# Performance work log

Measured on AMD Instinct MI355X. Metric: run time of the kernel, lower is better.

The kernel has to match this reference:

```python
import jax, jax.numpy as jnp
import numpy as np

HEADS = 16
KV_HEADS = 4
HEAD_DIM = 64
EMBED = 1024


def setup_inputs() -> dict:
    key = jax.random.key(0)
    k1, k2, k3, k4, k5 = jax.random.split(key, 5)
    B, S, G, E = 1, 2048, 2, EMBED
    scale = 1.0 / np.sqrt(E)
    x = jax.random.normal(k1, (B, S, G, E), dtype=jnp.float32)
    Wq = jax.random.normal(k2, (E, HEADS * HEAD_DIM), dtype=jnp.float32) * scale
    Wk = jax.random.normal(k3, (E, KV_HEADS * HEAD_DIM), dtype=jnp.float32) * scale
    Wv = jax.random.normal(k4, (E, KV_HEADS * HEAD_DIM), dtype=jnp.float32) * scale
    Wo = jax.random.normal(k5, (E, E), dtype=jnp.float32) * scale
    return {"x": x, "Wq": Wq, "Wk": Wk, "Wv": Wv, "Wo": Wo}


def reference(x, Wq, Wk, Wv, Wo):
    B, S, G, E = x.shape
    ratio = HEADS // KV_HEADS
    # projections over last dim (no bias, no activation)
    q = (x @ Wq).reshape(B, S, G, HEADS, HEAD_DIM)
    k = (x @ Wk).reshape(B, S, G, KV_HEADS, HEAD_DIM)
    v = (x @ Wv).reshape(B, S, G, KV_HEADS, HEAD_DIM)
    # GQA repeat_kv: each kv head repeated `ratio` times consecutively
    k = jnp.repeat(k, ratio, axis=3)  # [B,S,G,H,D]
    v = jnp.repeat(v, ratio, axis=3)
    # energy: [B,G,H,Q,K]
    energy = jnp.einsum('bqghd,bkghd->bghqk', q, k)
    # causal mask: triu(1) set to -inf (before the sqrt scaling, as in source)
    causal = jnp.triu(jnp.ones((S, S), dtype=bool), 1)
    energy = jnp.where(causal, -jnp.inf, energy)
    scores = jax.nn.softmax(energy / np.sqrt(HEAD_DIM), axis=-1)
    attn = jnp.einsum('bghqv,bvghd->bqghd', scores, v)
    attn = attn.reshape(B, S, G, E)
    return attn @ Wo
```

## Files before the change

kernel.cpp:

```cpp
#include <hip/hip_runtime.h>
#include <cstdint>
#include <cstddef>

typedef __bf16 bf16_t;
typedef bf16_t bf16x8 __attribute__((ext_vector_type(8)));
typedef float f32x4 __attribute__((ext_vector_type(4)));

__device__ inline bf16x8 load8(const float* p) {
  f32x4 a = *reinterpret_cast<const f32x4*>(p);
  f32x4 b = *reinterpret_cast<const f32x4*>(p + 4);
  bf16x8 r;
  r[0] = (bf16_t)a[0]; r[1] = (bf16_t)a[1];
  r[2] = (bf16_t)a[2]; r[3] = (bf16_t)a[3];
  r[4] = (bf16_t)b[0]; r[5] = (bf16_t)b[1];
  r[6] = (bf16_t)b[2]; r[7] = (bf16_t)b[3];
  return r;
}
__device__ inline bf16x8 load8(const bf16_t* p) {
  return *reinterpret_cast<const bf16x8*>(p);
}

__global__ __launch_bounds__(256) void cvtx_k(const float* __restrict__ x,
                                              bf16_t* __restrict__ xb) {
  const size_t i = (size_t)blockIdx.x * 2048 + (size_t)threadIdx.x * 8;
  *reinterpret_cast<bf16x8*>(xb + i) = load8(x + i);
}

__global__ __launch_bounds__(256) void cvtT_k(
    const float* __restrict__ Wq, const float* __restrict__ Wk,
    const float* __restrict__ Wv, const float* __restrict__ Wo,
    bf16_t* __restrict__ wqT, bf16_t* __restrict__ wkT,
    bf16_t* __restrict__ wvT, bf16_t* __restrict__ woT) {
  __shared__ bf16_t Ts[64][72];
  const int b = blockIdx.x;
  const float* S;
  bf16_t* D;
  int N, idx;
  if (b < 256) { S = Wq; D = wqT; N = 1024; idx = b; }
  else if (b < 320) { S = Wk; D = wkT; N = 256; idx = b - 256; }
  else if (b < 384) { S = Wv; D = wvT; N = 256; idx = b - 320; }
  else { S = Wo; D = woT; N = 1024; idx = b - 384; }
  const int ntl = (N == 1024) ? 4 : 2;
  const int kt0 = (idx >> ntl) * 64;
  const int n0 = (idx & ((1 << ntl) - 1)) * 64;
  const int tid = threadIdx.x;
#pragma unroll
  for (int i = 0; i < 2; ++i) {
    const int c = tid + 256 * i;
    const int row = c >> 3, col0 = (c & 7) * 8;
    *reinterpret_cast<bf16x8*>(&Ts[row][col0]) =
        load8(&S[(size_t)(kt0 + row) * N + n0 + col0]);
  }
  __syncthreads();
#pragma unroll
  for (int i = 0; i < 2; ++i) {
    const int c = tid + 256 * i;
    const int nrow = c >> 3, k0 = (c & 7) * 8;
    bf16x8 v;
#pragma unroll
    for (int j = 0; j < 8; ++j) v[j] = Ts[k0 + j][nrow];
    *reinterpret_cast<bf16x8*>(&D[(size_t)(n0 + nrow) * 1024 + kt0 + k0]) = v;
  }
}

template <typename OutT>
__device__ inline void gemm_bt_body(const bf16_t* __restrict__ A,
                                    const bf16_t* __restrict__ BT,
                                    OutT* __restrict__ C, int m0, int bt0,
                                    int K, int CN, int cn0, float alpha) {
  __shared__ __align__(16) bf16_t As[128][40];
  __shared__ __align__(16) bf16_t Bs[128][40];

  const int tid = threadIdx.x;
  const int wave = tid >> 6, lane = tid & 63;
  const int quad = lane >> 4, l16 = lane & 15;
  const int moff = (wave & 1) * 64, noff = (wave >> 1) * 64;

  f32x4 acc[4][4];
#pragma unroll
  for (int mt = 0; mt < 4; ++mt)
#pragma unroll
    for (int nt = 0; nt < 4; ++nt) acc[mt][nt] = {0.f, 0.f, 0.f, 0.f};

  const int arow = tid >> 1, ak0 = (tid & 1) * 16;

  bf16x8 a0, a1, b0, b1;
  {
    const bf16_t* ap = &A[(size_t)(m0 + arow) * K + ak0];
    a0 = load8(ap); a1 = load8(ap + 8);
    const bf16_t* bp = &BT[(size_t)(bt0 + arow) * K + ak0];
    b0 = load8(bp); b1 = load8(bp + 8);
  }

  for (int k0 = 0; k0 < K; k0 += 32) {
    *reinterpret_cast<bf16x8*>(&As[arow][ak0]) = a0;
    *reinterpret_cast<bf16x8*>(&As[arow][ak0 + 8]) = a1;
    *reinterpret_cast<bf16x8*>(&Bs[arow][ak0]) = b0;
    *reinterpret_cast<bf16x8*>(&Bs[arow][ak0 + 8]) = b1;
    __syncthreads();
    if (k0 + 32 < K) {
      const bf16_t* ap = &A[(size_t)(m0 + arow) * K + k0 + 32 + ak0];
      a0 = load8(ap); a1 = load8(ap + 8);
      const bf16_t* bp = &BT[(size_t)(bt0 + arow) * K + k0 + 32 + ak0];
      b0 = load8(bp); b1 = load8(bp + 8);
    }
    bf16x8 af[4], bfr[4];
#pragma unroll
    for (int mt = 0; mt < 4; ++mt)
      af[mt] =
          *reinterpret_cast<const bf16x8*>(&As[moff + mt * 16 + l16][quad * 8]);
#pragma unroll
    for (int nt = 0; nt < 4; ++nt)
      bfr[nt] =
          *reinterpret_cast<const bf16x8*>(&Bs[noff + nt * 16 + l16][quad * 8]);
#pragma unroll
    for (int mt = 0; mt < 4; ++mt)
#pragma unroll
      for (int nt = 0; nt < 4; ++nt)
        acc[mt][nt] = __builtin_amdgcn_mfma_f32_16x16x32_bf16(
            af[mt], bfr[nt], acc[mt][nt], 0, 0, 0);
    __syncthreads();
  }

#pragma unroll
  for (int mt = 0; mt < 4; ++mt) {
    const int crow = m0 + moff + mt * 16 + quad * 4;
#pragma unroll
    for (int nt = 0; nt < 4; ++nt) {
      const int ccol = cn0 + noff + nt * 16 + l16;
#pragma unroll
      for (int r = 0; r < 4; ++r)
        C[(size_t)(crow + r) * CN + ccol] = (OutT)(acc[mt][nt][r] * alpha);
    }
  }
}

__global__ __launch_bounds__(256, 3) void qkv_k(
    const bf16_t* __restrict__ x, const bf16_t* __restrict__ wqT,
    const bf16_t* __restrict__ wkT, const bf16_t* __restrict__ wvT,
    bf16_t* __restrict__ Qo, bf16_t* __restrict__ Ko, bf16_t* __restrict__ Vo) {
  const int n0 = blockIdx.x * 128;
  const int m0 = blockIdx.y * 128;
  const bf16_t* BT;
  bf16_t* C;
  int CN, bn0;
  float alpha;
  if (n0 < 1024) {
    BT = wqT; C = Qo; CN = 1024; bn0 = n0; alpha = 0.125f;
  } else if (n0 < 1280) {
    BT = wkT; C = Ko; CN = 256; bn0 = n0 - 1024; alpha = 1.0f;
  } else {
    BT = wvT; C = Vo; CN = 256; bn0 = n0 - 1280; alpha = 1.0f;
  }
  gemm_bt_body<bf16_t>(x, BT, C, m0, bn0, 1024, CN, bn0, alpha);
}

template <typename OutT>
__global__ __launch_bounds__(256, 3) void gemm_bt_k(
    const bf16_t* __restrict__ A, const bf16_t* __restrict__ BT,
    OutT* __restrict__ C, int K, int N, float alpha) {
  gemm_bt_body<OutT>(A, BT, C, blockIdx.y * 128, blockIdx.x * 128, K, N,
                     blockIdx.x * 128, alpha);
}

__global__ __launch_bounds__(256) void transpose_v_k(
    const bf16_t* __restrict__ V, bf16_t* __restrict__ VT) {
  __shared__ bf16_t Vs[64][72];
  const int tid = threadIdx.x;
  const int kt0 = blockIdx.x * 64;
  const int ghk = blockIdx.y;
  const int g = ghk >> 2, kh = ghk & 3;
#pragma unroll
  for (int i = 0; i < 2; ++i) {
    const int c = tid + 256 * i;
    const int row = c >> 3, d0 = (c & 7) * 8;
    *reinterpret_cast<bf16x8*>(&Vs[row][d0]) = *reinterpret_cast<const bf16x8*>(
        &V[((size_t)(kt0 + row) * 2 + g) * 256 + kh * 64 + d0]);
  }
  __syncthreads();
#pragma unroll
  for (int i = 0; i < 2; ++i) {
    const int c = tid + 256 * i;
    const int d = c >> 3, k0 = (c & 7) * 8;
    bf16x8 v;
#pragma unroll
    for (int j = 0; j < 8; ++j) v[j] = Vs[k0 + j][d];
    *reinterpret_cast<bf16x8*>(&VT[((size_t)ghk * 64 + d) * 2048 + kt0 + k0]) =
        v;
  }
}

__global__ __launch_bounds__(256, 4) void flash10_k(
    const bf16_t* __restrict__ Q, const bf16_t* __restrict__ K,
    const bf16_t* __restrict__ VT, bf16_t* __restrict__ ATTN) {
  __shared__ __align__(16) bf16_t Ks[64][64];
  __shared__ __align__(16) bf16_t Vs[64][64];
  __shared__ __align__(16) bf16_t Ps[4][16][64];

  const int tid = threadIdx.x;
  const int w = tid >> 6, lane = tid & 63;
  const int quad = lane >> 4, l16 = lane & 15;
  const int b = blockIdx.x;
  const int gh = blockIdx.y;
  const int j8 = b & 7;
  const int i8e = ((b >> 3) + (gh >> 3)) & 3;
  const int T = (i8e == 0) ? j8
              : (i8e == 1) ? (15 - j8)
              : (i8e == 2) ? (16 + j8)
                           : (31 - j8);
  const int g = gh >> 4, h = gh & 15, kh = h >> 2;
  const int qrow0 = T * 64 + w * 16;
  const int swz = ((l16 >> 2) & 3) << 4;
  const int rsw = l16 & 7;

  bf16x8 qf[2];
#pragma unroll
  for (int t = 0; t < 2; ++t)
    qf[t] = *reinterpret_cast<const bf16x8*>(
        &Q[((size_t)(qrow0 + l16) * 2 + g) * 1024 + h * 64 + t * 32 +
           quad * 8]);

  f32x4 O[4];
  f32x4 lp = {0.f, 0.f, 0.f, 0.f};
#pragma unroll
  for (int d = 0; d < 4; ++d) O[d] = {0.f, 0.f, 0.f, 0.f};

  bf16x8 kr[2], vr[2];
#pragma unroll
  for (int i = 0; i < 2; ++i) {
    const int c = tid + 256 * i;
    const int row = c >> 3, e0 = (c & 7) * 8;
    kr[i] = *reinterpret_cast<const bf16x8*>(
        &K[((size_t)(row)*2 + g) * 256 + kh * 64 + e0]);
    vr[i] = *reinterpret_cast<const bf16x8*>(
        &VT[((size_t)(g * 4 + kh) * 64 + row) * 2048 + e0]);
  }

  for (int kt = 0; kt <= T; ++kt) {
#pragma unroll
    for (int i = 0; i < 2; ++i) {
      const int c = tid + 256 * i;
      const int row = c >> 3;
      const int pb = (((c & 7) ^ (row & 7)) << 3);
      *reinterpret_cast<bf16x8*>(&Ks[row][pb]) = kr[i];
      *reinterpret_cast<bf16x8*>(&Vs[row][pb]) = vr[i];
    }
    __syncthreads();
    if (kt < T) {
      const int nt0 = (kt + 1) * 64;
#pragma unroll
      for (int i = 0; i < 2; ++i) {
        const int c = tid + 256 * i;
        const int row = c >> 3, e0 = (c & 7) * 8;
        kr[i] = *reinterpret_cast<const bf16x8*>(
            &K[((size_t)(nt0 + row) * 2 + g) * 256 + kh * 64 + e0]);
        vr[i] = *reinterpret_cast<const bf16x8*>(
            &VT[((size_t)(g * 4 + kh) * 64 + row) * 2048 + nt0 + e0]);
      }
    }

    f32x4 s[4];
    __builtin_amdgcn_s_setprio(1);
#pragma unroll
    for (int nt = 0; nt < 4; ++nt) {
      bf16x8 kf0 = *reinterpret_cast<const bf16x8*>(
          &Ks[nt * 16 + l16][(quad ^ rsw) << 3]);
      bf16x8 kf1 = *reinterpret_cast<const bf16x8*>(
          &Ks[nt * 16 + l16][((4 + quad) ^ rsw) << 3]);
      f32x4 z = {0.f, 0.f, 0.f, 0.f};
      z = __builtin_amdgcn_mfma_f32_16x16x32_bf16(qf[0], kf0, z, 0, 0, 0);
      s[nt] = __builtin_amdgcn_mfma_f32_16x16x32_bf16(qf[1], kf1, z, 0, 0, 0);
    }
    __builtin_amdgcn_s_setprio(0);
    const bool diag = (kt == T);
    const int qloc = w * 16 + quad * 4;
#pragma unroll
    for (int nt = 0; nt < 4; ++nt) {
      const int key = nt * 16 + l16;
#pragma unroll
      for (int r = 0; r < 4; ++r) {
        float p = __expf(s[nt][r]);
        if (diag && key > qloc + r) p = 0.f;
        lp[r] += p;
        Ps[w][quad * 4 + r][((nt ^ quad) << 4) + l16] = (bf16_t)p;
      }
    }
    bf16x8 pf[2];
#pragma unroll
    for (int t = 0; t < 2; ++t)
      pf[t] = *reinterpret_cast<const bf16x8*>(
          &Ps[w][l16][(t * 32 + quad * 8) ^ swz]);
    __builtin_amdgcn_s_setprio(1);
#pragma unroll
    for (int dnt = 0; dnt < 4; ++dnt) {
      bf16x8 vf0 = *reinterpret_cast<const bf16x8*>(
          &Vs[dnt * 16 + l16][(quad ^ rsw) << 3]);
      bf16x8 vf1 = *reinterpret_cast<const bf16x8*>(
          &Vs[dnt * 16 + l16][((4 + quad) ^ rsw) << 3]);
      O[dnt] = __builtin_amdgcn_mfma_f32_16x16x32_bf16(pf[0], vf0, O[dnt], 0,
                                                       0, 0);
      O[dnt] = __builtin_amdgcn_mfma_f32_16x16x32_bf16(pf[1], vf1, O[dnt], 0,
                                                       0, 0);
    }
    __builtin_amdgcn_s_setprio(0);
    __syncthreads();
  }

#pragma unroll
  for (int off = 1; off < 16; off <<= 1)
#pragma unroll
    for (int r = 0; r < 4; ++r) lp[r] += __shfl_xor(lp[r], off, 64);
#pragma unroll
  for (int r = 0; r < 4; ++r) {
    const float inv = 1.f / lp[r];
    const int row = qrow0 + quad * 4 + r;
#pragma unroll
    for (int dnt = 0; dnt < 4; ++dnt)
      ATTN[((size_t)row * 2 + g) * 1024 + h * 64 + dnt * 16 + l16] =
          (bf16_t)(O[dnt][r] * inv);
  }
}

extern "C" void kernel_launch(void* const* d_in, const int* in_sizes, int n_in,
                              void* d_out, int out_size, void* d_ws,
                              size_t ws_size, hipStream_t stream) {
  (void)in_sizes;
  (void)n_in;
  (void)out_size;
  (void)ws_size;

  const float* x = (const float*)d_in[0];
  const float* Wq = (const float*)d_in[1];
  const float* Wk = (const float*)d_in[2];
  const float* Wv = (const float*)d_in[3];
  const float* Wo = (const float*)d_in[4];
  float* out = (float*)d_out;

  const size_t MB = 1024 * 1024;
  char* ob = (char*)d_out;
  bf16_t* Qtmp = (bf16_t*)ob;
  bf16_t* VTws = (bf16_t*)(ob + 8 * MB);
  bf16_t* wqT = (bf16_t*)(ob + 10 * MB);
  bf16_t* wkT = (bf16_t*)(ob + 12 * MB);
  bf16_t* wvT = (bf16_t*)(ob + 12 * MB + 512 * 1024);
  bf16_t* Vws = (bf16_t*)(ob + 13 * MB);
  char* wb = (char*)d_ws;
  bf16_t* Kws = (bf16_t*)wb;
  bf16_t* woT = (bf16_t*)(wb + 2 * MB);
  bf16_t* ATTNws = (bf16_t*)(wb + 4 * MB);
  bf16_t* xb = ATTNws;

  cvtx_k<<<dim3(2048), dim3(256), 0, stream>>>(x, xb);
  cvtT_k<<<dim3(640), dim3(256), 0, stream>>>(Wq, Wk, Wv, Wo, wqT, wkT, wvT,
                                              woT);
  qkv_k<<<dim3(12, 32), dim3(256), 0, stream>>>(xb, wqT, wkT, wvT, Qtmp, Kws,
                                                Vws);
  transpose_v_k<<<dim3(32, 8), dim3(256), 0, stream>>>(Vws, VTws);
  flash10_k<<<dim3(32, 32), dim3(256), 0, stream>>>(Qtmp, Kws, VTws, ATTNws);
  gemm_bt_k<float><<<dim3(8, 32), dim3(256), 0, stream>>>(ATTNws, woT, out,
                                                          1024, 1024, 1.0f);
}
```

Before: 169.7 us.

## Stage GEMM tiles with direct global-to-LDS loads into swizzled double buffers

The shared bf16 GEMM body now copies A and B tiles straight from global memory into LDS with 16-byte global_load_lds, instead of loading into registers and then storing to LDS. LDS is double-buffered, so the next tile's load is issued while the current tile feeds the MFMAs, and one barrier per k-step is removed. The padded layout is replaced by an XOR swizzle on 8-element chunks to avoid bank conflicts. The risk is whether the compiler inserts the vmcnt wait needed for the async LDS writes before the barrier; doubled LDS may also affect occupancy.

```diff
diff --git a/kernel.cpp b/kernel.cpp
--- a/kernel.cpp
+++ b/kernel.cpp
@@ -18,6 +18,12 @@
 }
 __device__ inline bf16x8 load8(const bf16_t* p) {
   return *reinterpret_cast<const bf16x8*>(p);
+}
+
+__device__ inline void gload_lds16(const bf16_t* g, bf16_t* l) {
+  __builtin_amdgcn_global_load_lds(
+      (const __attribute__((address_space(1))) void*)g,
+      (__attribute__((address_space(3))) void*)l, 16, 0, 0);
 }
 
 __global__ __launch_bounds__(256) void cvtx_k(const float* __restrict__ x,
@@ -63,13 +69,24 @@
   }
 }
 
+__device__ inline void stage_glds(const bf16_t* __restrict__ G, int grow0,
+                                  int gK, int k0, bf16_t* lds, int w, int l) {
+#pragma unroll
+  for (int i = 0; i < 2; ++i) {
+    const int seg = w * 2 + i;
+    const int r = (seg << 4) + (l >> 2);
+    const int cb = (l & 3) ^ ((r >> 1) & 3);
+    gload_lds16(G + (size_t)(grow0 + r) * gK + k0 + cb * 8, lds + (seg << 9));
+  }
+}
+
 template <typename OutT>
 __device__ inline void gemm_bt_body(const bf16_t* __restrict__ A,
                                     const bf16_t* __restrict__ BT,
                                     OutT* __restrict__ C, int m0, int bt0,
                                     int K, int CN, int cn0, float alpha) {
-  __shared__ __align__(16) bf16_t As[128][40];
-  __shared__ __align__(16) bf16_t Bs[128][40];
+  __shared__ __align__(16) bf16_t As[2][128][32];
+  __shared__ __align__(16) bf16_t Bs[2][128][32];
 
   const int tid = threadIdx.x;
   const int wave = tid >> 6, lane = tid & 63;
@@ -82,44 +99,35 @@
 #pragma unroll
     for (int nt = 0; nt < 4; ++nt) acc[mt][nt] = {0.f, 0.f, 0.f, 0.f};
 
-  const int arow = tid >> 1, ak0 = (tid & 1) * 16;
-
-  bf16x8 a0, a1, b0, b1;
-  {
-    const bf16_t* ap = &A[(size_t)(m0 + arow) * K + ak0];
-    a0 = load8(ap); a1 = load8(ap + 8);
-    const bf16_t* bp = &BT[(size_t)(bt0 + arow) * K + ak0];
-    b0 = load8(bp); b1 = load8(bp + 8);
-  }
+  stage_glds(A, m0, K, 0, &As[0][0][0], wave, lane);
+  stage_glds(BT, bt0, K, 0, &Bs[0][0][0], wave, lane);
 
   for (int k0 = 0; k0 < K; k0 += 32) {
-    *reinterpret_cast<bf16x8*>(&As[arow][ak0]) = a0;
-    *reinterpret_cast<bf16x8*>(&As[arow][ak0 + 8]) = a1;
-    *reinterpret_cast<bf16x8*>(&Bs[arow][ak0]) = b0;
-    *reinterpret_cast<bf16x8*>(&Bs[arow][ak0 + 8]) = b1;
+    const int c = (k0 >> 5) & 1;
     __syncthreads();
     if (k0 + 32 < K) {
-      const bf16_t* ap = &A[(size_t)(m0 + arow) * K + k0 + 32 + ak0];
-      a0 = load8(ap); a1 = load8(ap + 8);
-      const bf16_t* bp = &BT[(size_t)(bt0 + arow) * K + k0 + 32 + ak0];
-      b0 = load8(bp); b1 = load8(bp + 8);
+      stage_glds(A, m0, K, k0 + 32, &As[c ^ 1][0][0], wave, lane);
+      stage_glds(BT, bt0, K, k0 + 32, &Bs[c ^ 1][0][0], wave, lane);
     }
     bf16x8 af[4], bfr[4];
 #pragma unroll
-    for (int mt = 0; mt < 4; ++mt)
-      af[mt] =
-          *reinterpret_cast<const bf16x8*>(&As[moff + mt * 16 + l16][quad * 8]);
-#pragma unroll
-    for (int nt = 0; nt < 4; ++nt)
-      bfr[nt] =
-          *reinterpret_cast<const bf16x8*>(&Bs[noff + nt * 16 + l16][quad * 8]);
+    for (int mt = 0; mt < 4; ++mt) {
+      const int row = moff + mt * 16 + l16;
+      af[mt] = *reinterpret_cast<const bf16x8*>(
+          &As[c][row][(quad ^ ((row >> 1) & 3)) * 8]);
+    }
+#pragma unroll
+    for (int nt = 0; nt < 4; ++nt) {
+      const int row = noff + nt * 16 + l16;
+      bfr[nt] = *reinterpret_cast<const bf16x8*>(
+          &Bs[c][row][(quad ^ ((row >> 1) & 3)) * 8]);
+    }
 #pragma unroll
     for (int mt = 0; mt < 4; ++mt)
 #pragma unroll
       for (int nt = 0; nt < 4; ++nt)
         acc[mt][nt] = __builtin_amdgcn_mfma_f32_16x16x32_bf16(
             af[mt], bfr[nt], acc[mt][nt], 0, 0, 0);
-    __syncthreads();
   }
 
 #pragma unroll
```

Result: faster. 166.3 us (-2.1%).
